# Kernel tuning notes

Hardware: AMD Instinct MI355X
Metric: run time of the kernel (lower is better)

## Reference

```python
import jax, jax.numpy as jnp
import numpy as np

N, E, G = 50000, 600000, 256
D, L, V = 128, 5, 128
BN_EPS = 1e-5


def setup_inputs() -> dict:
    key = jax.random.key(0)
    ks = jax.random.split(key, 24)
    x = jax.random.randint(ks[0], (N, 9), 0, V)
    edge_index = jax.random.randint(ks[1], (2, E), 0, N)
    edge_attr = jax.random.randint(ks[2], (E, 3), 0, V)
    batch = jnp.sort(jax.random.randint(ks[3], (N,), 0, G))
    s = 0.02
    inp = dict(
        x=x, edge_index=edge_index, edge_attr=edge_attr, batch=batch,
        atom_emb=jax.random.normal(ks[4], (9, V, D)) * s,
        bond_emb=jax.random.normal(ks[5], (L, 3, V, D)) * s,
        eps=jnp.zeros((L,)),
        W1=jax.random.normal(ks[6], (D, 2 * D)) * s, b1=jnp.zeros((2 * D,)),
        g1=jnp.ones((2 * D,)), be1=jnp.zeros((2 * D,)),
        W2=jax.random.normal(ks[7], (2 * D, D)) * s, b2=jnp.zeros((D,)),
        bn_g=jnp.ones((L, D)), bn_b=jnp.zeros((L, D)),
        fcW1=jax.random.normal(ks[8], (D, 1024)) * s, fcb1=jnp.zeros((1024,)),
        fcW2=jax.random.normal(ks[9], (1024, 1024)) * s, fcb2=jnp.zeros((1024,)),
        fcW3=jax.random.normal(ks[10], (1024, 512)) * s, fcb3=jnp.zeros((512,)),
        fcW4=jax.random.normal(ks[11], (512, 1)) * s, fcb4=jnp.zeros((1,)),
    )
    return inp


def _bn(h, g, b):
    # training-mode batchnorm (biased variance, as torch uses for normalization)
    m = h.mean(0)
    v = jnp.var(h, axis=0)
    return (h - m) * jax.lax.rsqrt(v + BN_EPS) * g + b


def _embed(tables, idx):
    # tables: [F, V, D], idx: [M, F] -> sum over F of table lookups -> [M, D]
    F = tables.shape[0]
    return tables[jnp.arange(F)[None, :], idx].sum(axis=1)


def reference(x, edge_index, edge_attr, batch, atom_emb, bond_emb, eps,
              W1, b1, g1, be1, W2, b2, bn_g, bn_b,
              fcW1, fcb1, fcW2, fcb2, fcW3, fcb3, fcW4, fcb4):
    src, dst = edge_index[0], edge_index[1]

    def mlp(h):
        z = jax.nn.relu(_bn(h @ W1 + b1, g1, be1))
        return z @ W2 + b2

    h = _embed(atom_emb, x)  # AtomEncoder: [N, D]
    h_sum = h  # JK='sum' accumulator
    for l in range(L):
        e = _embed(bond_emb[l], edge_attr)            # BondEncoder: [E, D]
        msg = jax.nn.relu(h[src] + e)                  # gather + elementwise
        agg = jax.ops.segment_sum(msg, dst, num_segments=N)  # scatter-add
        h = mlp((1.0 + eps[l]) * h + agg)
        h = _bn(h, bn_g[l], bn_b[l])
        if l < L - 1:
            h = jax.nn.relu(h)
        # dropout is identity in eval mode
        h_sum = h_sum + h

    # global mean pool over graphs
    sums = jax.ops.segment_sum(h_sum, batch, num_segments=G)
    cnts = jax.ops.segment_sum(jnp.ones((N,), h_sum.dtype), batch, num_segments=G)
    rep = sums / jnp.maximum(cnts, 1.0)[:, None]

    z = jax.nn.relu(rep @ fcW1 + fcb1)
    z = jax.nn.relu(z @ fcW2 + fcb2)
    z = jax.nn.relu(z @ fcW3 + fcb3)
    out = (z @ fcW4 + fcb4).squeeze(-1)  # [G]
    return out
```

## Files before the change

### kernel.cpp

```cpp
#include <hip/hip_runtime.h>

typedef unsigned short u16;
typedef unsigned int u32;
typedef __bf16 bf16x8 __attribute__((ext_vector_type(8)));
typedef float f32x4 __attribute__((ext_vector_type(4)));

#define NN 50000
#define EE 600000
#define GG 256
#define LL 5
#define NB 196

__device__ __forceinline__ float b2f(u16 u) {
  unsigned int v = ((unsigned int)u) << 16;
  return __builtin_bit_cast(float, v);
}
__device__ __forceinline__ u16 f2b(float f) {
  unsigned int u = __builtin_bit_cast(unsigned int, f);
  u += 0x7FFFu + ((u >> 16) & 1u);
  return (u16)(u >> 16);
}

__global__ void k_detect(const u32* __restrict__ w, int* __restrict__ flag) {
  __shared__ int sh[256];
  u32 v = w[threadIdx.x];
  u32 lo = v & 0xFFFFu;
  u32 e = (lo >> 7) & 0xFFu;
  sh[threadIdx.x] = (e >= 0x60u && e <= 0x7Fu) ? 1 : 0;
  __syncthreads();
  for (int s = 128; s > 0; s >>= 1) {
    if (threadIdx.x < (unsigned)s) sh[threadIdx.x] += sh[threadIdx.x + s];
    __syncthreads();
  }
  if (threadIdx.x == 0) flag[0] = (sh[0] < 128) ? 1 : 0;
}

struct CvtArgs {
  const void* src[19];
  u16* dst[19];
  int cum[20];
};

__global__ void k_cvt_all(CvtArgs a, const int* __restrict__ flag) {
  int t = blockIdx.x * 256 + threadIdx.x;
  if (t >= a.cum[19]) return;
  int i = 0;
  while (t >= a.cum[i + 1]) ++i;
  int j = t - a.cum[i];
  if (flag[0]) a.dst[i][j] = f2b(((const float*)a.src[i])[j]);
  else a.dst[i][j] = ((const u16*)a.src[i])[j];
}

__global__ void k_tr(const u16* __restrict__ src, u16* __restrict__ dst, int K, int N) {
  int idx = blockIdx.x * 256 + threadIdx.x;
  if (idx >= K * N) return;
  int n = idx / K, k = idx - n * K;
  dst[idx] = src[k * N + n];
}

__global__ void k_deg(const int* __restrict__ ei, int* __restrict__ deg) {
  int e = blockIdx.x * 256 + threadIdx.x;
  if (e < EE) atomicAdd(&deg[ei[EE + e]], 1);
}

__global__ void k_scan1(const int* __restrict__ deg, int* __restrict__ rowp,
                        int* __restrict__ bsum) {
  __shared__ int sh[256];
  int i = blockIdx.x * 256 + threadIdx.x;
  int v = (i < NN) ? deg[i] : 0;
  sh[threadIdx.x] = v;
  __syncthreads();
  for (int s = 1; s < 256; s <<= 1) {
    int t = (threadIdx.x >= (unsigned)s) ? sh[threadIdx.x - s] : 0;
    __syncthreads();
    sh[threadIdx.x] += t;
    __syncthreads();
  }
  if (i < NN) rowp[i] = sh[threadIdx.x] - v;
  if (threadIdx.x == 255) bsum[blockIdx.x] = sh[255];
}

__global__ void k_scan2(int* __restrict__ bsum, int* __restrict__ boff) {
  __shared__ int sh[256];
  int v = (threadIdx.x < NB) ? bsum[threadIdx.x] : 0;
  sh[threadIdx.x] = v;
  __syncthreads();
  for (int s = 1; s < 256; s <<= 1) {
    int t = (threadIdx.x >= (unsigned)s) ? sh[threadIdx.x - s] : 0;
    __syncthreads();
    sh[threadIdx.x] += t;
    __syncthreads();
  }
  if (threadIdx.x < NB) boff[threadIdx.x] = sh[threadIdx.x] - v;
}

__global__ void k_scan3(int* __restrict__ rowp, const int* __restrict__ boff,
                        int* __restrict__ cursor) {
  int i = blockIdx.x * 256 + threadIdx.x;
  if (i < NN) {
    int r = rowp[i] + boff[blockIdx.x];
    rowp[i] = r;
    cursor[i] = r;
  }
  if (i == 0) rowp[NN] = EE;
}

__global__ void k_fill(const int* __restrict__ ei, const int* __restrict__ eattr,
                       int* __restrict__ cursor, uint2* __restrict__ epack) {
  int e = blockIdx.x * 256 + threadIdx.x;
  if (e < EE) {
    int d = ei[EE + e];
    int pos = atomicAdd(&cursor[d], 1);
    u32 src = (u32)ei[e];
    u32 a0 = (u32)eattr[e * 3], a1 = (u32)eattr[e * 3 + 1], a2 = (u32)eattr[e * 3 + 2];
    epack[pos] = make_uint2(src | (a0 << 16) | (a1 << 23), a2);
  }
}

__global__ void k_gb(const int* __restrict__ batch, int* __restrict__ gstart,
                     int* __restrict__ gend) {
  int n = blockIdx.x * 256 + threadIdx.x;
  if (n < NN) {
    int b = batch[n];
    atomicMin(&gstart[b], n);
    atomicMax(&gend[b], n);
  }
}

__global__ void k_atom(const int* __restrict__ x, const u16* __restrict__ aemb,
                       u16* __restrict__ h) {
  int idx = blockIdx.x * 256 + threadIdx.x;
  if (idx >= NN * 64) return;
  int n = idx >> 6, f2 = (idx & 63) << 1;
  float a0 = 0.f, a1 = 0.f;
#pragma unroll
  for (int j = 0; j < 9; ++j) {
    int xv = x[n * 9 + j];
    u32 v = *(const u32*)(aemb + (j * 128 + xv) * 128 + f2);
    a0 += b2f((u16)v);
    a1 += b2f((u16)(v >> 16));
  }
  u32 o = (u32)f2b(a0) | ((u32)f2b(a1) << 16);
  *(u32*)(h + n * 128 + f2) = o;
}

__global__ __launch_bounds__(256)
void k_pull(const u16* __restrict__ h, const int* __restrict__ rowp,
            const uint2* __restrict__ epack, const u16* __restrict__ bond,
            const u16* __restrict__ epsv, int layer, u16* __restrict__ amat) {
  const int lane = threadIdx.x & 63;
  const int node = blockIdx.x * 4 + (threadIdx.x >> 6);
  const int p0 = rowp[node], p1 = rowp[node + 1];
  const int lo = lane << 1;
  const u16* bondB = bond + 16384;
  const u16* bondC = bond + 32768;
  float acc0 = 0.f, acc1 = 0.f;
  int p = p0;
  for (; p + 4 <= p1; p += 4) {
    uint2 e0 = epack[p], e1 = epack[p + 1], e2 = epack[p + 2], e3 = epack[p + 3];
    u32 h0 = *(const u32*)(h + (size_t)(e0.x & 0xFFFFu) * 128 + lo);
    u32 h1 = *(const u32*)(h + (size_t)(e1.x & 0xFFFFu) * 128 + lo);
    u32 h2 = *(const u32*)(h + (size_t)(e2.x & 0xFFFFu) * 128 + lo);
    u32 h3 = *(const u32*)(h + (size_t)(e3.x & 0xFFFFu) * 128 + lo);
    u32 a0 = *(const u32*)(bond + ((e0.x >> 16) & 0x7Fu) * 128 + lo);
    u32 a1 = *(const u32*)(bond + ((e1.x >> 16) & 0x7Fu) * 128 + lo);
    u32 a2 = *(const u32*)(bond + ((e2.x >> 16) & 0x7Fu) * 128 + lo);
    u32 a3 = *(const u32*)(bond + ((e3.x >> 16) & 0x7Fu) * 128 + lo);
    u32 b0 = *(const u32*)(bondB + ((e0.x >> 23) & 0x7Fu) * 128 + lo);
    u32 b1 = *(const u32*)(bondB + ((e1.x >> 23) & 0x7Fu) * 128 + lo);
    u32 b2 = *(const u32*)(bondB + ((e2.x >> 23) & 0x7Fu) * 128 + lo);
    u32 b3 = *(const u32*)(bondB + ((e3.x >> 23) & 0x7Fu) * 128 + lo);
    u32 c0 = *(const u32*)(bondC + e0.y * 128 + lo);
    u32 c1 = *(const u32*)(bondC + e1.y * 128 + lo);
    u32 c2 = *(const u32*)(bondC + e2.y * 128 + lo);
    u32 c3 = *(const u32*)(bondC + e3.y * 128 + lo);
    acc0 += fmaxf(b2f((u16)h0) + b2f((u16)a0) + b2f((u16)b0) + b2f((u16)c0), 0.f);
    acc1 += fmaxf(b2f((u16)(h0 >> 16)) + b2f((u16)(a0 >> 16)) + b2f((u16)(b0 >> 16)) + b2f((u16)(c0 >> 16)), 0.f);
    acc0 += fmaxf(b2f((u16)h1) + b2f((u16)a1) + b2f((u16)b1) + b2f((u16)c1), 0.f);
    acc1 += fmaxf(b2f((u16)(h1 >> 16)) + b2f((u16)(a1 >> 16)) + b2f((u16)(b1 >> 16)) + b2f((u16)(c1 >> 16)), 0.f);
    acc0 += fmaxf(b2f((u16)h2) + b2f((u16)a2) + b2f((u16)b2) + b2f((u16)c2), 0.f);
    acc1 += fmaxf(b2f((u16)(h2 >> 16)) + b2f((u16)(a2 >> 16)) + b2f((u16)(b2 >> 16)) + b2f((u16)(c2 >> 16)), 0.f);
    acc0 += fmaxf(b2f((u16)h3) + b2f((u16)a3) + b2f((u16)b3) + b2f((u16)c3), 0.f);
    acc1 += fmaxf(b2f((u16)(h3 >> 16)) + b2f((u16)(a3 >> 16)) + b2f((u16)(b3 >> 16)) + b2f((u16)(c3 >> 16)), 0.f);
  }
  for (; p < p1; ++p) {
    uint2 e0 = epack[p];
    u32 h0 = *(const u32*)(h + (size_t)(e0.x & 0xFFFFu) * 128 + lo);
    u32 a0 = *(const u32*)(bond + ((e0.x >> 16) & 0x7Fu) * 128 + lo);
    u32 b0 = *(const u32*)(bondB + ((e0.x >> 23) & 0x7Fu) * 128 + lo);
    u32 c0 = *(const u32*)(bondC + e0.y * 128 + lo);
    acc0 += fmaxf(b2f((u16)h0) + b2f((u16)a0) + b2f((u16)b0) + b2f((u16)c0), 0.f);
    acc1 += fmaxf(b2f((u16)(h0 >> 16)) + b2f((u16)(a0 >> 16)) + b2f((u16)(b0 >> 16)) + b2f((u16)(c0 >> 16)), 0.f);
  }
  float epsf = 1.0f + b2f(epsv[layer]);
  u32 own = *(const u32*)(h + (size_t)node * 128 + lo);
  u32 o = (u32)f2b(epsf * b2f((u16)own) + acc0) |
          ((u32)f2b(epsf * b2f((u16)(own >> 16)) + acc1) << 16);
  *(u32*)(amat + (size_t)node * 128 + lo) = o;
}

__global__ __launch_bounds__(256)
void k_gemm1(const u16* __restrict__ amat, const u16* __restrict__ w1t,
             const u16* __restrict__ b1, u16* __restrict__ z0,
             float* __restrict__ bnsum, float* __restrict__ bnsq) {
  __shared__ u16 As[128 * 72];
  __shared__ u16 Bs[128 * 72];
  __shared__ float colAcc[256];
  const int tid = threadIdx.x;
  const int r0 = blockIdx.x * 128;
  const int nc = blockIdx.y * 128;
  const int w = tid >> 6, lane = tid & 63, l15 = lane & 15, q = lane >> 4;
  const int wr = (w & 1) * 64, wc = (w >> 1) * 64;
  f32x4 acc[4][4];
#pragma unroll
  for (int i = 0; i < 4; ++i)
#pragma unroll
    for (int j = 0; j < 4; ++j) acc[i][j] = {0.f, 0.f, 0.f, 0.f};

#pragma unroll
  for (int ks = 0; ks < 2; ++ks) {
    const int k0 = ks * 64;
    for (int idx = tid; idx < 1024; idx += 256) {
      const int row = idx >> 3, c8 = (idx & 7) << 3;
      int gr = r0 + row; if (gr >= NN) gr = NN - 1;
      uint4 va = *(const uint4*)(amat + (size_t)gr * 128 + k0 + c8);
      *(uint4*)(As + row * 72 + c8) = va;
      uint4 vb = *(const uint4*)(w1t + (size_t)(nc + row) * 128 + k0 + c8);
      *(uint4*)(Bs + row * 72 + c8) = vb;
    }
    __syncthreads();
#pragma unroll
    for (int kk = 0; kk < 64; kk += 32) {
      const int kf = kk + q * 8;
      bf16x8 a[4], b[4];
#pragma unroll
      for (int i = 0; i < 4; ++i) a[i] = *(const bf16x8*)(As + (wr + i * 16 + l15) * 72 + kf);
#pragma unroll
      for (int j = 0; j < 4; ++j) b[j] = *(const bf16x8*)(Bs + (wc + j * 16 + l15) * 72 + kf);
#pragma unroll
      for (int i = 0; i < 4; ++i)
#pragma unroll
        for (int j = 0; j < 4; ++j)
          acc[i][j] = __builtin_amdgcn_mfma_f32_16x16x32_bf16(a[i], b[j], acc[i][j], 0, 0, 0);
    }
    __syncthreads();
  }
  colAcc[tid] = 0.f;
  __syncthreads();
#pragma unroll
  for (int j = 0; j < 4; ++j) {
    const int c = wc + j * 16 + l15;
    const float bias = b2f(b1[nc + c]);
    float ls = 0.f, lsq = 0.f;
#pragma unroll
    for (int i = 0; i < 4; ++i) {
      const int gr = r0 + wr + i * 16 + q * 4;
#pragma unroll
      for (int rg = 0; rg < 4; ++rg) {
        if (gr + rg < NN) {
          const float v = acc[i][j][rg] + bias;
          z0[(gr + rg) * 256 + nc + c] = f2b(v);
          ls += v;
          lsq += v * v;
        }
      }
    }
    atomicAdd(&colAcc[c], ls);
    atomicAdd(&colAcc[128 + c], lsq);
  }
  __syncthreads();
  if (tid < 128) {
    atomicAdd(&bnsum[nc + tid], colAcc[tid]);
    atomicAdd(&bnsq[nc + tid], colAcc[128 + tid]);
  }
}

__global__ void k_bnfin(float* __restrict__ bnsum, float* __restrict__ bnsq,
                        const u16* __restrict__ g, const u16* __restrict__ b,
                        float* __restrict__ c1, float* __restrict__ c0) {
  int t = threadIdx.x;
  float s = bnsum[t], q = bnsq[t];
  bnsum[t] = 0.f;
  bnsq[t] = 0.f;
  float m = s * (1.0f / NN);
  float var = q * (1.0f / NN) - m * m;
  float rs = rsqrtf(var + 1e-5f);
  float cc1 = rs * b2f(g[t]);
  c1[t] = cc1;
  c0[t] = b2f(b[t]) - m * cc1;
}

__global__ __launch_bounds__(256)
void k_gemm2(const u16* __restrict__ z0, const float* __restrict__ c1,
             const float* __restrict__ c0, const u16* __restrict__ w2t,
             const u16* __restrict__ b2, u16* __restrict__ hpre,
             float* __restrict__ bnsum, float* __restrict__ bnsq) {
  __shared__ u16 As[128 * 72];
  __shared__ u16 Bs[128 * 72];
  __shared__ float colAcc[256];
  const int tid = threadIdx.x;
  const int r0 = blockIdx.x * 128;
  const int w = tid >> 6, lane = tid & 63, l15 = lane & 15, q = lane >> 4;
  const int wr = (w & 1) * 64, wc = (w >> 1) * 64;
  f32x4 acc[4][4];
#pragma unroll
  for (int i = 0; i < 4; ++i)
#pragma unroll
    for (int j = 0; j < 4; ++j) acc[i][j] = {0.f, 0.f, 0.f, 0.f};

#pragma unroll
  for (int ks = 0; ks < 4; ++ks) {
    const int k0 = ks * 64;
    for (int idx = tid; idx < 1024; idx += 256) {
      const int row = idx >> 3, c8 = (idx & 7) << 3;
      int gr = r0 + row; if (gr >= NN) gr = NN - 1;
      ushort4 z01 = *(const ushort4*)(z0 + (size_t)gr * 256 + k0 + c8);
      ushort4 z23 = *(const ushort4*)(z0 + (size_t)gr * 256 + k0 + c8 + 4);
      ushort4 o01, o23;
      {
        const int k = k0 + c8;
        o01.x = f2b(fmaxf(b2f(z01.x) * c1[k + 0] + c0[k + 0], 0.f));
        o01.y = f2b(fmaxf(b2f(z01.y) * c1[k + 1] + c0[k + 1], 0.f));
        o01.z = f2b(fmaxf(b2f(z01.z) * c1[k + 2] + c0[k + 2], 0.f));
        o01.w = f2b(fmaxf(b2f(z01.w) * c1[k + 3] + c0[k + 3], 0.f));
        o23.x = f2b(fmaxf(b2f(z23.x) * c1[k + 4] + c0[k + 4], 0.f));
        o23.y = f2b(fmaxf(b2f(z23.y) * c1[k + 5] + c0[k + 5], 0.f));
        o23.z = f2b(fmaxf(b2f(z23.z) * c1[k + 6] + c0[k + 6], 0.f));
        o23.w = f2b(fmaxf(b2f(z23.w) * c1[k + 7] + c0[k + 7], 0.f));
      }
      *(ushort4*)(As + row * 72 + c8) = o01;
      *(ushort4*)(As + row * 72 + c8 + 4) = o23;
      uint4 vb = *(const uint4*)(w2t + (size_t)row * 256 + k0 + c8);
      *(uint4*)(Bs + row * 72 + c8) = vb;
    }
    __syncthreads();
#pragma unroll
    for (int kk = 0; kk < 64; kk += 32) {
      const int kf = kk + q * 8;
      bf16x8 a[4], b[4];
#pragma unroll
      for (int i = 0; i < 4; ++i) a[i] = *(const bf16x8*)(As + (wr + i * 16 + l15) * 72 + kf);
#pragma unroll
      for (int j = 0; j < 4; ++j) b[j] = *(const bf16x8*)(Bs + (wc + j * 16 + l15) * 72 + kf);
#pragma unroll
      for (int i = 0; i < 4; ++i)
#pragma unroll
        for (int j = 0; j < 4; ++j)
          acc[i][j] = __builtin_amdgcn_mfma_f32_16x16x32_bf16(a[i], b[j], acc[i][j], 0, 0, 0);
    }
    __syncthreads();
  }
  colAcc[tid] = 0.f;
  __syncthreads();
#pragma unroll
  for (int j = 0; j < 4; ++j) {
    const int c = wc + j * 16 + l15;
    const float bias = b2f(b2[c]);
    float ls = 0.f, lsq = 0.f;
#pragma unroll
    for (int i = 0; i < 4; ++i) {
      const int gr = r0 + wr + i * 16 + q * 4;
#pragma unroll
      for (int rg = 0; rg < 4; ++rg) {
        if (gr + rg < NN) {
          const float v = acc[i][j][rg] + bias;
          hpre[(gr + rg) * 128 + c] = f2b(v);
          ls += v;
          lsq += v * v;
        }
      }
    }
    atomicAdd(&colAcc[c], ls);
    atomicAdd(&colAcc[128 + c], lsq);
  }
  __syncthreads();
  if (tid < 128) {
    atomicAdd(&bnsum[tid], colAcc[tid]);
    atomicAdd(&bnsq[tid], colAcc[128 + tid]);
  }
}

__global__ void k_bnapply(const u16* __restrict__ hpre, const float* __restrict__ c1,
                          const float* __restrict__ c0, u16* __restrict__ h, int dorelu) {
  int idx4 = (blockIdx.x * 256 + threadIdx.x) * 4;
  if (idx4 >= NN * 128) return;
  int f = idx4 & 127;
  const ushort4 hv = *(const ushort4*)(hpre + idx4);
  const float4 rv = *(const float4*)(c1 + f);
  const float4 bv = *(const float4*)(c0 + f);
  float v0 = b2f(hv.x) * rv.x + bv.x;
  float v1 = b2f(hv.y) * rv.y + bv.y;
  float v2 = b2f(hv.z) * rv.z + bv.z;
  float v3 = b2f(hv.w) * rv.w + bv.w;
  if (dorelu) {
    v0 = fmaxf(v0, 0.f); v1 = fmaxf(v1, 0.f);
    v2 = fmaxf(v2, 0.f); v3 = fmaxf(v3, 0.f);
  }
  ushort4 ov;
  ov.x = f2b(v0); ov.y = f2b(v1); ov.z = f2b(v2); ov.w = f2b(v3);
  *(ushort4*)(h + idx4) = ov;
}

__global__ void k_poolseg(const u16* __restrict__ h, const int* __restrict__ gstart,
                          const int* __restrict__ gend, float* __restrict__ rep) {
  int g = blockIdx.x >> 2, part = blockIdx.x & 3, f = threadIdx.x;
  int r0 = gstart[g], r1 = gend[g] + 1;
  int len = r1 - r0;
  if (len <= 0) return;
  int chunk = (len + 3) >> 2;
  int s = r0 + part * chunk;
  int e = s + chunk; if (e > r1) e = r1;
  float acc = 0.f;
  for (int r = s; r < e; ++r) acc += b2f(h[r * 128 + f]);
  if (s < e) atomicAdd(&rep[g * 128 + f], acc);
}

__global__ void k_rep(float* __restrict__ rep, const int* __restrict__ gstart,
                      const int* __restrict__ gend, u16* __restrict__ repb) {
  int idx = blockIdx.x * 256 + threadIdx.x;
  int g = idx >> 7;
  int c = gend[g] - gstart[g] + 1;
  if (c < 1) c = 1;
  float v = rep[idx] / (float)c;
  rep[idx] = v;
  repb[idx] = f2b(v);
}

__global__ __launch_bounds__(256)
void k_fcg(const u16* __restrict__ A, const u16* __restrict__ Wt,
           const u16* __restrict__ bias, u16* __restrict__ out, int K, int N) {
  const int tid = threadIdx.x;
  const int r0 = blockIdx.x * 128;
  const int nc = blockIdx.y * 128;
  const int w = tid >> 6, lane = tid & 63, l15 = lane & 15, q = lane >> 4;
  const int wr = (w & 1) * 64, wc = (w >> 1) * 64;
  f32x4 acc[4][4];
#pragma unroll
  for (int i = 0; i < 4; ++i)
#pragma unroll
    for (int j = 0; j < 4; ++j) acc[i][j] = {0.f, 0.f, 0.f, 0.f};
  const int nkb = K >> 5;
  for (int kb = 0; kb < nkb; ++kb) {
    const int kf = kb * 32 + q * 8;
    bf16x8 a[4], b[4];
#pragma unroll
    for (int i = 0; i < 4; ++i)
      a[i] = *(const bf16x8*)(A + (size_t)(r0 + wr + i * 16 + l15) * K + kf);
#pragma unroll
    for (int j = 0; j < 4; ++j)
      b[j] = *(const bf16x8*)(Wt + (size_t)(nc + wc + j * 16 + l15) * K + kf);
#pragma unroll
    for (int i = 0; i < 4; ++i)
#pragma unroll
      for (int j = 0; j < 4; ++j)
        acc[i][j] = __builtin_amdgcn_mfma_f32_16x16x32_bf16(a[i], b[j], acc[i][j], 0, 0, 0);
  }
#pragma unroll
  for (int j = 0; j < 4; ++j) {
    const int c = nc + wc + j * 16 + l15;
    const float bv = b2f(bias[c]);
#pragma unroll
    for (int i = 0; i < 4; ++i) {
      const int gr = r0 + wr + i * 16 + q * 4;
#pragma unroll
      for (int rg = 0; rg < 4; ++rg)
        out[(gr + rg) * N + c] = f2b(fmaxf(acc[i][j][rg] + bv, 0.f));
    }
  }
}

__global__ void k_fc4(const u16* __restrict__ z, const u16* __restrict__ W,
                      const u16* __restrict__ bias, void* __restrict__ out,
                      const int* __restrict__ flag) {
  int g = blockIdx.x, lane = threadIdx.x;
  float acc = 0.f;
  for (int k = lane; k < 512; k += 64) acc += b2f(z[g * 512 + k]) * b2f(W[k]);
  for (int off = 32; off > 0; off >>= 1) acc += __shfl_down(acc, off);
  if (lane == 0) {
    float r = acc + b2f(bias[0]);
    if (flag[0]) ((float*)out)[g] = r;
    else ((u16*)out)[g] = f2b(r);
  }
}

extern "C" void kernel_launch(void* const* d_in, const int* in_sizes, int n_in,
                              void* d_out, int out_size, void* d_ws, size_t ws_size,
                              hipStream_t stream) {
  const int* x     = (const int*)d_in[0];
  const int* ei    = (const int*)d_in[1];
  const int* eattr = (const int*)d_in[2];
  const int* batch = (const int*)d_in[3];

  char* ws = (char*)d_ws;
  size_t off = 0;
  auto alloc = [&](size_t bytes) -> void* {
    void* p = ws + off;
    off += (bytes + 255) & ~(size_t)255;
    return p;
  };
  int* flag = (int*)alloc(256);
  u16* cvt[23];
  CvtArgs ca;
  ca.cum[0] = 0;
  for (int i = 4; i <= 22; ++i) {
    cvt[i] = (u16*)alloc((size_t)in_sizes[i] * 2);
    ca.src[i - 4] = d_in[i];
    ca.dst[i - 4] = cvt[i];
    ca.cum[i - 3] = ca.cum[i - 4] + in_sizes[i];
  }

  u16*   h      = (u16*)  alloc((size_t)NN * 128 * 2);
  u16*   amat   = (u16*)  alloc((size_t)NN * 128 * 2);
  u16*   z0     = (u16*)  alloc((size_t)NN * 256 * 2);
  u16*   w1t    = (u16*)  alloc(32768 * 2);
  u16*   w2t    = (u16*)  alloc(32768 * 2);
  u16*   ft1    = (u16*)  alloc((size_t)1024 * 128 * 2);
  u16*   ft2    = (u16*)  alloc((size_t)1024 * 1024 * 2);
  u16*   ft3    = (u16*)  alloc((size_t)512 * 1024 * 2);
  int*   deg    = (int*)  alloc((size_t)NN * 4);
  int*   cursor = (int*)  alloc((size_t)NN * 4);
  int*   rowp   = (int*)  alloc((size_t)(NN + 1) * 4);
  int*   bsum   = (int*)  alloc((size_t)NB * 4);
  int*   boff   = (int*)  alloc((size_t)NB * 4);
  uint2* epack  = (uint2*)alloc((size_t)EE * 8);
  float* bnbuf  = (float*)alloc(768 * 4);
  float* bnstat = (float*)alloc(1152 * 4);
  float* rep    = (float*)alloc((size_t)GG * 128 * 4);
  u16*   repb   = (u16*)  alloc((size_t)GG * 128 * 2);
  int*   gstart = (int*)  alloc((size_t)GG * 4);
  int*   gend   = (int*)  alloc((size_t)GG * 4);
  u16*   fz1    = (u16*)  alloc((size_t)GG * 1024 * 2);
  u16*   fz2    = (u16*)  alloc((size_t)GG * 1024 * 2);
  u16*   fz3    = (u16*)  alloc((size_t)GG * 512 * 2);
  (void)ws_size; (void)n_in; (void)out_size;

  u16* hpre = amat;

  float* bn1sum = bnbuf;
  float* bn1sq  = bnbuf + 256;
  float* bn2sum = bnbuf + 512;
  float* bn2sq  = bnbuf + 640;
  float* c1a    = bnstat;
  float* c0a    = bnstat + 256;
  float* c1b    = bnstat + 512;
  float* c0b    = bnstat + 640;

  k_detect<<<1, 256, 0, stream>>>((const u32*)d_in[4], flag);
  {
    int total = ca.cum[19];
    k_cvt_all<<<(total + 255) / 256, 256, 0, stream>>>(ca, flag);
  }
  const u16 *aembc = cvt[4], *bembc = cvt[5], *epsc = cvt[6], *w1c = cvt[7],
            *b1c = cvt[8], *g1c = cvt[9], *be1c = cvt[10], *w2c = cvt[11],
            *b2c = cvt[12], *bngc = cvt[13], *bnbc = cvt[14], *fw1 = cvt[15],
            *fb1 = cvt[16], *fw2 = cvt[17], *fb2 = cvt[18], *fw3 = cvt[19],
            *fb3 = cvt[20], *fw4 = cvt[21], *fb4 = cvt[22];

  k_tr<<<128, 256, 0, stream>>>(w1c, w1t, 128, 256);
  k_tr<<<128, 256, 0, stream>>>(w2c, w2t, 256, 128);
  k_tr<<<512, 256, 0, stream>>>(fw1, ft1, 128, 1024);
  k_tr<<<4096, 256, 0, stream>>>(fw2, ft2, 1024, 1024);
  k_tr<<<2048, 256, 0, stream>>>(fw3, ft3, 1024, 512);

  hipMemsetAsync(deg, 0, (size_t)NN * 4, stream);
  hipMemsetAsync(rep, 0, (size_t)GG * 128 * 4, stream);
  hipMemsetAsync(gstart, 0x7F, (size_t)GG * 4, stream);
  hipMemsetAsync(gend, 0xFF, (size_t)GG * 4, stream);
  hipMemsetAsync(bnbuf, 0, 768 * 4, stream);
  k_deg<<<(EE + 255) / 256, 256, 0, stream>>>(ei, deg);
  k_scan1<<<NB, 256, 0, stream>>>(deg, rowp, bsum);
  k_scan2<<<1, 256, 0, stream>>>(bsum, boff);
  k_scan3<<<NB, 256, 0, stream>>>(rowp, boff, cursor);
  k_fill<<<(EE + 255) / 256, 256, 0, stream>>>(ei, eattr, cursor, epack);
  k_gb<<<(NN + 255) / 256, 256, 0, stream>>>(batch, gstart, gend);
  k_atom<<<(NN * 64 + 255) / 256, 256, 0, stream>>>(x, aembc, h);
  k_poolseg<<<GG * 4, 128, 0, stream>>>(h, gstart, gend, rep);

  const int gx = (NN + 127) / 128;
  for (int l = 0; l < LL; ++l) {
    k_pull<<<(NN + 3) / 4, 256, 0, stream>>>(h, rowp, epack,
                                             bembc + (size_t)l * 3 * 128 * 128, epsc, l, amat);
    dim3 grid1(gx, 2);
    k_gemm1<<<grid1, 256, 0, stream>>>(amat, w1t, b1c, z0, bn1sum, bn1sq);
    k_bnfin<<<1, 256, 0, stream>>>(bn1sum, bn1sq, g1c, be1c, c1a, c0a);
    k_gemm2<<<gx, 256, 0, stream>>>(z0, c1a, c0a, w2t, b2c, hpre, bn2sum, bn2sq);
    k_bnfin<<<1, 128, 0, stream>>>(bn2sum, bn2sq, bngc + l * 128, bnbc + l * 128,
                                   c1b, c0b);
    k_bnapply<<<(NN * 128) / 1024, 256, 0, stream>>>(hpre, c1b, c0b, h,
                                                     (l < LL - 1) ? 1 : 0);
    k_poolseg<<<GG * 4, 128, 0, stream>>>(h, gstart, gend, rep);
  }

  k_rep<<<(GG * 128) / 256, 256, 0, stream>>>(rep, gstart, gend, repb);
  {
    dim3 g1(2, 8), g2(2, 8), g3(2, 4);
    k_fcg<<<g1, 256, 0, stream>>>(repb, ft1, fb1, fz1, 128, 1024);
    k_fcg<<<g2, 256, 0, stream>>>(fz1, ft2, fb2, fz2, 1024, 1024);
    k_fcg<<<g3, 256, 0, stream>>>(fz2, ft3, fb3, fz3, 1024, 512);
  }
  k_fc4<<<GG, 64, 0, stream>>>(fz3, fw4, fb4, d_out, flag);
}
```

Baseline: 1.028 ms.

## Tile weight transposes, fuse memsets into one init kernel, simplify graph bounds

Weight transposes now go through a 32x32 shared-memory tile, so both the reads and the writes are coalesced instead of the strided reads of the old version. Five hipMemsetAsync calls are merged into a single init kernel to cut launch overhead. Graph start and end are found by comparing neighbours in the sorted batch array, which removes the atomics. Both GEMMs get a min-blocks hint of 2 in launch_bounds, which may limit registers. gstart is initialised to 0 instead of a large value, so an empty graph would get start 0 and end -1; this is harmless if the pooling loop skips ranges where start is after end.

Result: faster. 940.4 us (-8.5%).

```diff
diff --git a/kernel.cpp b/kernel.cpp
--- a/kernel.cpp
+++ b/kernel.cpp
@@ -52,10 +52,24 @@
 }
 
 __global__ void k_tr(const u16* __restrict__ src, u16* __restrict__ dst, int K, int N) {
-  int idx = blockIdx.x * 256 + threadIdx.x;
-  if (idx >= K * N) return;
-  int n = idx / K, k = idx - n * K;
-  dst[idx] = src[k * N + n];
+  __shared__ u16 t[32][33];
+  const int kb = blockIdx.x * 32, nb = blockIdx.y * 32;
+  const int tx = threadIdx.x & 31, ty = threadIdx.x >> 5;
+#pragma unroll
+  for (int i = ty; i < 32; i += 8) t[i][tx] = src[(kb + i) * N + nb + tx];
+  __syncthreads();
+#pragma unroll
+  for (int i = ty; i < 32; i += 8) dst[(nb + i) * K + kb + tx] = t[tx][i];
+}
+
+__global__ void k_init(int* __restrict__ deg, float* __restrict__ rep,
+                       float* __restrict__ bnbuf, int* __restrict__ gstart,
+                       int* __restrict__ gend) {
+  int i = blockIdx.x * 256 + threadIdx.x;
+  if (i < NN) deg[i] = 0;
+  if (i < GG * 128) rep[i] = 0.f;
+  if (i < 768) bnbuf[i] = 0.f;
+  if (i < GG) { gstart[i] = 0; gend[i] = -1; }
 }
 
 __global__ void k_deg(const int* __restrict__ ei, int* __restrict__ deg) {
@@ -120,11 +134,10 @@
 __global__ void k_gb(const int* __restrict__ batch, int* __restrict__ gstart,
                      int* __restrict__ gend) {
   int n = blockIdx.x * 256 + threadIdx.x;
-  if (n < NN) {
-    int b = batch[n];
-    atomicMin(&gstart[b], n);
-    atomicMax(&gend[b], n);
-  }
+  if (n >= NN) return;
+  int b = batch[n];
+  if (n == 0 || batch[n - 1] != b) gstart[b] = n;
+  if (n == NN - 1 || batch[n + 1] != b) gend[b] = n;
 }
 
 __global__ void k_atom(const int* __restrict__ x, const u16* __restrict__ aemb,
@@ -199,7 +212,7 @@
   *(u32*)(amat + (size_t)node * 128 + lo) = o;
 }
 
-__global__ __launch_bounds__(256)
+__global__ __launch_bounds__(256, 2)
 void k_gemm1(const u16* __restrict__ amat, const u16* __restrict__ w1t,
              const u16* __restrict__ b1, u16* __restrict__ z0,
              float* __restrict__ bnsum, float* __restrict__ bnsq) {
@@ -290,7 +303,7 @@
   c0[t] = b2f(b[t]) - m * cc1;
 }
 
-__global__ __launch_bounds__(256)
+__global__ __launch_bounds__(256, 2)
 void k_gemm2(const u16* __restrict__ z0, const float* __restrict__ c1,
              const float* __restrict__ c0, const u16* __restrict__ w2t,
              const u16* __restrict__ b2, u16* __restrict__ hpre,
@@ -556,17 +569,16 @@
             *fb1 = cvt[16], *fw2 = cvt[17], *fb2 = cvt[18], *fw3 = cvt[19],
             *fb3 = cvt[20], *fw4 = cvt[21], *fb4 = cvt[22];
 
-  k_tr<<<128, 256, 0, stream>>>(w1c, w1t, 128, 256);
-  k_tr<<<128, 256, 0, stream>>>(w2c, w2t, 256, 128);
-  k_tr<<<512, 256, 0, stream>>>(fw1, ft1, 128, 1024);
-  k_tr<<<4096, 256, 0, stream>>>(fw2, ft2, 1024, 1024);
-  k_tr<<<2048, 256, 0, stream>>>(fw3, ft3, 1024, 512);
-
-  hipMemsetAsync(deg, 0, (size_t)NN * 4, stream);
-  hipMemsetAsync(rep, 0, (size_t)GG * 128 * 4, stream);
-  hipMemsetAsync(gstart, 0x7F, (size_t)GG * 4, stream);
-  hipMemsetAsync(gend, 0xFF, (size_t)GG * 4, stream);
-  hipMemsetAsync(bnbuf, 0, 768 * 4, stream);
+  {
+    dim3 t1(4, 8), t2(8, 4), t3(4, 32), t4(32, 32), t5(32, 16);
+    k_tr<<<t1, 256, 0, stream>>>(w1c, w1t, 128, 256);
+    k_tr<<<t2, 256, 0, stream>>>(w2c, w2t, 256, 128);
+    k_tr<<<t3, 256, 0, stream>>>(fw1, ft1, 128, 1024);
+    k_tr<<<t4, 256, 0, stream>>>(fw2, ft2, 1024, 1024);
+    k_tr<<<t5, 256, 0, stream>>>(fw3, ft3, 1024, 512);
+  }
+
+  k_init<<<(NN + 255) / 256, 256, 0, stream>>>(deg, rep, bnbuf, gstart, gend);
   k_deg<<<(EE + 255) / 256, 256, 0, stream>>>(ei, deg);
   k_scan1<<<NB, 256, 0, stream>>>(deg, rowp, bsum);
   k_scan2<<<1, 256, 0, stream>>>(bsum, boff);
```
